# Kernel tuning notes

Hardware: AMD Instinct MI355X
Metric: run time of the kernel (lower is better)

## Reference

```python
import jax, jax.numpy as jnp
import numpy as np

B, L1, L2, D = 16, 512, 512, 512
H, INNER = 8, 1024
HD = INNER // H  # 128

def _glorot(key, shape):
    fan_in, fan_out = shape[-2], shape[-1]
    lim = jnp.sqrt(6.0 / (fan_in + fan_out))
    return jax.random.uniform(key, shape, jnp.float32, -lim, lim)

def setup_inputs() -> dict:
    key = jax.random.key(0)
    ks = jax.random.split(key, 8)
    return {
        "primary": jax.random.normal(ks[0], (B, L1, D), jnp.float32),
        "secondary": jax.random.normal(ks[1], (B, L2, D), jnp.float32),
        "primary_mask": jnp.ones((B, L1), jnp.float32),
        "secondary_mask": jnp.ones((B, L2), jnp.float32),
        "W_aff": _glorot(ks[2], (H, D, D)),          # per-head bilinear affinity weights
        "W_p": _glorot(ks[3], (D, INNER)),            # linear_primary (no bias)
        "W_s": _glorot(ks[4], (D, INNER)),            # linear_secondary (no bias)
        "W_fp": _glorot(ks[5], (D + HD, D)),          # ffn_primary
        "b_fp": jnp.zeros((D,), jnp.float32),
        "W_fs": _glorot(ks[6], (D + HD, D)),          # ffn_secondary
        "b_fs": jnp.zeros((D,), jnp.float32),
    }

def reference(primary, secondary, primary_mask, secondary_mask,
              W_aff, W_p, W_s, W_fp, b_fp, W_fs, b_fs):
    b, l1, d = primary.shape
    l2 = secondary.shape[1]
    h = W_aff.shape[0]
    hd = W_p.shape[1] // h
    # affinity mask: (B, 1, L1, L2)
    mask = (primary_mask[:, :, None] * secondary_mask[:, None, :])[:, None, :, :]
    # multi-head bilinear affinity: tanh(P Wk S^T) -> (B, H, L1, L2)
    aff = jnp.tanh(jnp.einsum('bie,hef,bjf->bhij', primary, W_aff, secondary)) * mask
    # project + split heads -> (B, H, L, hd)
    pp = (primary @ W_p).reshape(b, l1, h, hd).transpose(0, 2, 1, 3)
    ps = (secondary @ W_s).reshape(b, l2, h, hd).transpose(0, 2, 1, 3)
    # weighted sums (ReLU activation)
    wp = jax.nn.relu(jnp.einsum('bhij,bhid->bhjd', aff, pp))  # (B, H, L2, hd)
    ws = jax.nn.relu(jnp.einsum('bhij,bhjd->bhid', aff, ps))  # (B, H, L1, hd)
    # GlobalMaxPool1D applied to (L, H, hd) per sample => max over heads
    pool_p = wp.max(axis=1)  # (B, L2, hd)
    pool_s = ws.max(axis=1)  # (B, L1, hd)
    out_p = jax.nn.relu(jnp.concatenate([primary, pool_s], -1) @ W_fp + b_fp)
    out_s = jax.nn.relu(jnp.concatenate([secondary, pool_p], -1) @ W_fs + b_fs)
    return out_p, out_s
```

## Files before the change

kernel.cpp:

```cpp
#include <hip/hip_runtime.h>
#include <hip/hip_bf16.h>

typedef short short8 __attribute__((ext_vector_type(8)));
typedef float f32x16 __attribute__((ext_vector_type(16)));
typedef float f32x4 __attribute__((ext_vector_type(4)));

#define BM 128
#define BN 128

typedef const __attribute__((address_space(1))) void gas_t;
typedef __attribute__((address_space(3))) void las_t;

__device__ __forceinline__ unsigned short f2bf(float f) {
  unsigned int u = __float_as_uint(f);
  u += 0x7FFFu + ((u >> 16) & 1u);
  return (unsigned short)(u >> 16);
}

__device__ __forceinline__ float fast_tanh(float x) {
  x = fminf(fmaxf(x, -10.f), 10.f);
  float t = __builtin_amdgcn_exp2f(x * 2.8853900817779268f);
  return 1.f - 2.f * __builtin_amdgcn_rcpf(t + 1.f);
}

struct GemmP {
  const unsigned short* A;
  const unsigned short* Bm;
  void* C;
  const float* A2f;
  const unsigned short* A_b;
  const unsigned short* Bm_b;
  void* C_b;
  const float* A2f_b;
  const float* mask_p;
  const float* mask_s;
  const float* bias;
  const float* bias_b;
  long long sAb, sAh, sBb, sBh, sCb, sCh;
  int lda, lda2, ldb, ldc, M, N, K, Hh, kSplit, zSplit, nbx, nby;
};

template <int TA, int EPI>
__device__ __forceinline__ void gemm_body(const GemmP& p, int bx, int by, int bz, char* smem_) {
  constexpr int PA = (TA == 0) ? 32 : 40;
  constexpr int HSA = (TA == 0) ? 4096 : 5120;
  unsigned short* As = (unsigned short*)smem_;
  unsigned short* Bs = (unsigned short*)(smem_ + 2 * HSA * 2);

  int z = bz;
  const unsigned short* Abase = p.A;
  const unsigned short* Bbase = p.Bm;
  void* Cvp = p.C;
  const float* A2f = p.A2f;
  const float* bias = p.bias;
  if (p.zSplit && z >= p.zSplit) {
    z -= p.zSplit;
    Abase = p.A_b; Bbase = p.Bm_b; Cvp = p.C_b; A2f = p.A2f_b; bias = p.bias_b;
  }
  const int zb = z / p.Hh, zh = z % p.Hh;
  const unsigned short* A = Abase + (size_t)zb * p.sAb + (size_t)zh * p.sAh;
  const unsigned short* B = Bbase + (size_t)zb * p.sBb + (size_t)zh * p.sBh;
  const int m0 = bx * BM, n0 = by * BN;
  const int tid = threadIdx.x;
  const int wid = tid >> 6, lane = tid & 63;
  const int wm = (wid >> 1) * 64, wn = (wid & 1) * 64;
  const int lrow = lane & 31;
  const int lk8 = (lane >> 5) * 8;

  f32x16 acc[2][2] = {};

  const int dm = tid >> 2, dkg = tid & 3;

  auto mfma_block = [&]() {
#pragma unroll
    for (int h = 0; h < 2; ++h)
#pragma unroll
      for (int kc = 0; kc < 2; ++kc) {
        short8 af[2], bfv[2];
#pragma unroll
        for (int mt = 0; mt < 2; ++mt)
          af[mt] = *(const short8*)&As[h * HSA + (wm + mt * 32 + lrow) * PA + kc * 16 + lk8];
#pragma unroll
        for (int nt = 0; nt < 2; ++nt)
          bfv[nt] = *(const short8*)&Bs[h * 4096 + (wn + nt * 32 + lrow) * 32 + kc * 16 + lk8];
#pragma unroll
        for (int mt = 0; mt < 2; ++mt)
#pragma unroll
          for (int nt = 0; nt < 2; ++nt)
            acc[mt][nt] = __builtin_amdgcn_mfma_f32_32x32x16_bf16(af[mt], bfv[nt], acc[mt][nt], 0, 0, 0);
      }
  };
  auto stage_b = [&](int k0) {
#pragma unroll
    for (int h = 0; h < 2; ++h)
#pragma unroll
      for (int q = 0; q < 2; ++q) {
        const unsigned short* src = B + (size_t)(n0 + q * 64 + dm) * p.ldb + (k0 + h * 32 + dkg * 8);
        __builtin_amdgcn_global_load_lds((gas_t*)src,
                                         (las_t*)&Bs[h * 4096 + q * 2048 + wid * 512],
                                         16, 0, 0);
      }
  };

  const int nIter = p.K >> 6;
  const int nIter1 = p.kSplit ? (p.kSplit >> 6) : nIter;

  for (int it = 0; it < nIter1; ++it) {
    const int k0 = it << 6;
    if (TA == 0) {
#pragma unroll
      for (int h = 0; h < 2; ++h)
#pragma unroll
        for (int q = 0; q < 2; ++q) {
          const unsigned short* src = A + (size_t)(m0 + q * 64 + dm) * p.lda + (k0 + h * 32 + dkg * 8);
          __builtin_amdgcn_global_load_lds((gas_t*)src,
                                           (las_t*)&As[h * HSA + q * 2048 + wid * 512],
                                           16, 0, 0);
        }
    } else {
      const int kk = tid & 31, mg = (tid >> 5) << 4;
#pragma unroll
      for (int h = 0; h < 2; ++h) {
        const unsigned short* src = A + (size_t)(k0 + h * 32 + kk) * p.lda + (m0 + mg);
        uint4 v0 = *(const uint4*)src;
        uint4 v1 = *(const uint4*)(src + 8);
        unsigned short tmp[16];
        *(uint4*)&tmp[0] = v0;
        *(uint4*)&tmp[8] = v1;
#pragma unroll
        for (int j = 0; j < 16; ++j) As[h * HSA + (mg + j) * PA + kk] = tmp[j];
      }
    }
    stage_b(k0);
    __syncthreads();
    mfma_block();
    __syncthreads();
  }

  if (TA == 0 && p.kSplit) {
    for (int it = nIter1; it < nIter; ++it) {
      const int k0 = it << 6;
#pragma unroll
      for (int h = 0; h < 2; ++h) {
        const int ko = k0 + h * 32 - p.kSplit;
#pragma unroll
        for (int q = 0; q < 2; ++q) {
          const float* src = A2f + (size_t)(m0 + q * 64 + dm) * p.lda2 + (ko + dkg * 8);
          float4 v0 = *(const float4*)src;
          float4 v1 = *(const float4*)(src + 4);
          __attribute__((aligned(16))) unsigned short t[8];
          t[0] = f2bf(v0.x); t[1] = f2bf(v0.y); t[2] = f2bf(v0.z); t[3] = f2bf(v0.w);
          t[4] = f2bf(v1.x); t[5] = f2bf(v1.y); t[6] = f2bf(v1.z); t[7] = f2bf(v1.w);
          *(uint4*)&As[h * HSA + (q * 64 + dm) * 32 + dkg * 8] = *(const uint4*)t;
        }
      }
      stage_b(k0);
      __syncthreads();
      mfma_block();
      __syncthreads();
    }
  }

  unsigned short* Cu = (unsigned short*)Cvp + (size_t)zb * p.sCb + (size_t)zh * p.sCh;
  float* Cf = (float*)Cvp + (size_t)zb * p.sCb + (size_t)zh * p.sCh;

  const int rbase = 4 * (lane >> 5);

  float mp[2][16], ms[2];
  if constexpr (EPI == 1) {
#pragma unroll
    for (int mt = 0; mt < 2; ++mt)
#pragma unroll
      for (int reg = 0; reg < 16; ++reg) {
        const int rl = (reg & 3) + 8 * (reg >> 2) + rbase;
        mp[mt][reg] = p.mask_p[(size_t)zb * p.M + (m0 + wm + mt * 32 + rl)];
      }
#pragma unroll
    for (int nt = 0; nt < 2; ++nt)
      ms[nt] = p.mask_s[(size_t)zb * p.N + (n0 + wn + nt * 32 + lrow)];
  }
  if constexpr (EPI == 3) {
#pragma unroll
    for (int nt = 0; nt < 2; ++nt)
      ms[nt] = bias[n0 + wn + nt * 32 + lrow];
  }

#pragma unroll
  for (int mt = 0; mt < 2; ++mt) {
#pragma unroll
    for (int nt = 0; nt < 2; ++nt) {
      f32x16 a = acc[mt][nt];
#pragma unroll
      for (int reg = 0; reg < 16; ++reg) {
        const int rl = (reg & 3) + 8 * (reg >> 2) + rbase;
        const int grow = m0 + wm + mt * 32 + rl;
        const int gcol = n0 + wn + nt * 32 + lrow;
        const size_t idx = (size_t)grow * p.ldc + gcol;
        const float v = a[reg];
        if constexpr (EPI == 0) {
          Cu[idx] = f2bf(v);
        } else if constexpr (EPI == 1) {
          Cu[idx] = f2bf(fast_tanh(v) * (mp[mt][reg] * ms[nt]));
        } else if constexpr (EPI == 2) {
          atomicMax((int*)Cf + idx, __float_as_int(fmaxf(v, 0.f)));
        } else {
          Cf[idx] = fmaxf(v + ms[nt], 0.f);
        }
      }
    }
  }
}

template <int TA, int EPI>
__global__ __launch_bounds__(256) void gemm_k(GemmP p) {
  extern __shared__ char smem[];
  gemm_body<TA, EPI>(p, blockIdx.x, blockIdx.y, blockIdx.z, smem);
}

template <int TA1, int EPI1, int TA2, int EPI2>
__global__ __launch_bounds__(256) void gemm_pair_k(GemmP a, GemmP b, int nA) {
  extern __shared__ char smem[];
  int bid = blockIdx.x;
  if (bid < nA) {
    const int per = a.nbx * a.nby;
    const int z = bid / per, r = bid % per;
    gemm_body<TA1, EPI1>(a, r % a.nbx, r / a.nbx, z, smem);
  } else {
    bid -= nA;
    const int per = b.nbx * b.nby;
    const int z = bid / per, r = bid % per;
    gemm_body<TA2, EPI2>(b, r % b.nbx, r / b.nbx, z, smem);
  }
}

#define VMCNT6() asm volatile("s_waitcnt vmcnt(6)" ::: "memory")
#define VMCNT0() asm volatile("s_waitcnt vmcnt(0)" ::: "memory")

template <int EPI>
__device__ __forceinline__ void gemm8_body(const GemmP& p, int bx, int by, int bz, char* smem_) {
  int z = bz;
  const unsigned short* Abase = p.A;
  const unsigned short* Bbase = p.Bm;
  void* Cvp = p.C;
  if (p.zSplit && z >= p.zSplit) {
    z -= p.zSplit;
    Abase = p.A_b; Bbase = p.Bm_b; Cvp = p.C_b;
  }
  const int zb = z / p.Hh, zh = z % p.Hh;
  const unsigned short* A = Abase + (size_t)zb * p.sAb + (size_t)zh * p.sAh;
  const unsigned short* B = Bbase + (size_t)zb * p.sBb + (size_t)zh * p.sBh;
  const int m0 = bx * 256, n0 = by * 128;
  const int tid = threadIdx.x;
  const int wid = tid >> 6, lane = tid & 63;
  const int wm = wid >> 1, wn = wid & 1;
  const int lrow = lane & 15, lhi = lane >> 4;

  unsigned short* lds_u = (unsigned short*)smem_;

  const int rr = tid >> 3;
  const int cc = ((tid & 7) * 8) ^ ((rr & 7) << 3);

  const int laneA0 = (wm * 64 + lrow) * 128 + ((lhi * 16) ^ ((lrow & 7) << 4));
  const int laneB0 = (wn * 64 + lrow) * 128 + ((lhi * 16) ^ ((lrow & 7) << 4));

  f32x4 acc[4][4] = {};

  auto stageA = [&](int t, int slot) {
    const int k0 = t << 6;
    const unsigned short* s0 = A + (size_t)(m0 + rr) * p.lda + k0 + cc;
#pragma unroll
    for (int s = 0; s < 4; ++s)
      __builtin_amdgcn_global_load_lds((gas_t*)(s0 + (size_t)s * 64 * p.lda),
                                       (las_t*)(lds_u + slot * 24576 + s * 4096 + wid * 512),
                                       16, 0, 0);
  };
  auto stageB = [&](int t, int slot) {
    const int k0 = t << 6;
    const unsigned short* s0 = B + (size_t)(n0 + rr) * p.ldb + k0 + cc;
#pragma unroll
    for (int s = 0; s < 2; ++s)
      __builtin_amdgcn_global_load_lds((gas_t*)(s0 + (size_t)s * 64 * p.ldb),
                                       (las_t*)(lds_u + slot * 24576 + 16384 + s * 4096 + wid * 512),
                                       16, 0, 0);
  };

  const int nt = p.K >> 6;

  stageA(0, 0); stageB(0, 0);
  stageA(1, 1); stageB(1, 1);
  VMCNT6();
  __builtin_amdgcn_s_barrier();
  __builtin_amdgcn_sched_barrier(0);

  int slot = 0;
  for (int t = 0; t < nt; ++t) {
    const int s1 = (slot == 2) ? 0 : slot + 1;
    const int s2 = (s1 == 2) ? 0 : s1 + 1;
    const char* baseA0 = smem_ + slot * 49152 + laneA0;
    const char* baseA1 = smem_ + slot * 49152 + (laneA0 ^ 64);
    const char* baseB0 = smem_ + slot * 49152 + 32768 + laneB0;
    const char* baseB1 = smem_ + slot * 49152 + 32768 + (laneB0 ^ 64);
    short8 af[4], bv[4];

#pragma unroll
    for (int fm = 0; fm < 4; ++fm) af[fm] = *(const short8*)(baseA0 + fm * 2048);
#pragma unroll
    for (int fn = 0; fn < 4; ++fn) bv[fn] = *(const short8*)(baseB0 + fn * 2048);
    if (t + 2 < nt) stageA(t + 2, s2);
    __builtin_amdgcn_s_barrier();
    __builtin_amdgcn_sched_barrier(0);
    __builtin_amdgcn_s_setprio(1);
#pragma unroll
    for (int fm = 0; fm < 4; ++fm)
#pragma unroll
      for (int fn = 0; fn < 4; ++fn)
        acc[fm][fn] = __builtin_amdgcn_mfma_f32_16x16x32_bf16(af[fm], bv[fn], acc[fm][fn], 0, 0, 0);
    __builtin_amdgcn_s_setprio(0);
    __builtin_amdgcn_s_barrier();
    __builtin_amdgcn_sched_barrier(0);

#pragma unroll
    for (int fm = 0; fm < 4; ++fm) af[fm] = *(const short8*)(baseA1 + fm * 2048);
#pragma unroll
    for (int fn = 0; fn < 4; ++fn) bv[fn] = *(const short8*)(baseB1 + fn * 2048);
    if (t + 2 < nt) stageB(t + 2, s2);
    __builtin_amdgcn_s_barrier();
    __builtin_amdgcn_sched_barrier(0);
    __builtin_amdgcn_s_setprio(1);
#pragma unroll
    for (int fm = 0; fm < 4; ++fm)
#pragma unroll
      for (int fn = 0; fn < 4; ++fn)
        acc[fm][fn] = __builtin_amdgcn_mfma_f32_16x16x32_bf16(af[fm], bv[fn], acc[fm][fn], 0, 0, 0);
    __builtin_amdgcn_s_setprio(0);
    __builtin_amdgcn_sched_barrier(0);

    if (t + 1 < nt) {
      if (t + 2 < nt) VMCNT6(); else VMCNT0();
      __builtin_amdgcn_s_barrier();
      __builtin_amdgcn_sched_barrier(0);
    }
    slot = s1;
  }

  unsigned short* Cu = (unsigned short*)Cvp + (size_t)zb * p.sCb + (size_t)zh * p.sCh;

  float mp[4][4], ms[4];
  if constexpr (EPI == 1) {
#pragma unroll
    for (int fm = 0; fm < 4; ++fm)
#pragma unroll
      for (int reg = 0; reg < 4; ++reg)
        mp[fm][reg] = p.mask_p[(size_t)zb * p.M + (m0 + wm * 64 + fm * 16 + lhi * 4 + reg)];
#pragma unroll
    for (int fn = 0; fn < 4; ++fn)
      ms[fn] = p.mask_s[(size_t)zb * p.N + (n0 + wn * 64 + fn * 16 + lrow)];
  }

#pragma unroll
  for (int fm = 0; fm < 4; ++fm)
#pragma unroll
    for (int fn = 0; fn < 4; ++fn) {
      f32x4 a = acc[fm][fn];
      const int gcol = n0 + wn * 64 + fn * 16 + lrow;
#pragma unroll
      for (int reg = 0; reg < 4; ++reg) {
        const int grow = m0 + wm * 64 + fm * 16 + lhi * 4 + reg;
        const size_t idx = (size_t)grow * p.ldc + gcol;
        if constexpr (EPI == 0) Cu[idx] = f2bf(a[reg]);
        else                    Cu[idx] = f2bf(fast_tanh(a[reg]) * (mp[fm][reg] * ms[fn]));
      }
    }
}

template <int EPI>
__global__ __launch_bounds__(512, 2) void gemm8_k(GemmP p) {
  extern __shared__ char smem[];
  gemm8_body<EPI>(p, blockIdx.x, blockIdx.y, blockIdx.z, smem);
}

template <int E1, int E2>
__global__ __launch_bounds__(512, 2) void gemm8_pair_k(GemmP a, GemmP b, int nA) {
  extern __shared__ char smem[];
  int bid = blockIdx.x;
  if (bid < nA) {
    const int per = a.nbx * a.nby;
    const int z = bid / per, r = bid % per;
    gemm8_body<E1>(a, r % a.nbx, r / a.nbx, z, smem);
  } else {
    bid -= nA;
    const int per = b.nbx * b.nby;
    const int z = bid / per, r = bid % per;
    gemm8_body<E2>(b, r % b.nbx, r / b.nbx, z, smem);
  }
}

__device__ __forceinline__ void trans_body(const float* src, unsigned short* dst,
                                           int R, int C, int bx, int by, float (*tile)[33]) {
  const int r0 = by * 32, c0 = bx * 32;
  const int tx = threadIdx.x & 31, ty = threadIdx.x >> 5;
#pragma unroll
  for (int j = 0; j < 4; ++j)
    tile[ty + j * 8][tx] = src[(size_t)(r0 + ty + j * 8) * C + (c0 + tx)];
  __syncthreads();
#pragma unroll
  for (int j = 0; j < 4; ++j)
    dst[(size_t)(c0 + ty + j * 8) * R + (r0 + tx)] = f2bf(tile[tx][ty + j * 8]);
}

__global__ __launch_bounds__(256) void prep_k(const float* P, const float* S,
                                              unsigned short* Pbf, unsigned short* Sbf,
                                              const float* W_aff, unsigned short* WaT,
                                              const float* W_p, unsigned short* WpT,
                                              const float* W_s, unsigned short* WsT,
                                              const float* W_fp, unsigned short* WfpT,
                                              const float* W_fs, unsigned short* WfsT,
                                              float* poolz) {
  __shared__ float tile[32][33];
  const int bid = blockIdx.x;
  if (bid < 8192) {
    const int n4 = 1048576;
    int i = bid * 256 + threadIdx.x;
    const float4* s = (const float4*)P;
    ushort4* d = (ushort4*)Pbf;
    if (i >= n4) { i -= n4; s = (const float4*)S; d = (ushort4*)Sbf; }
    float4 v = s[i];
    ushort4 o;
    o.x = f2bf(v.x); o.y = f2bf(v.y); o.z = f2bf(v.z); o.w = f2bf(v.w);
    d[i] = o;
  } else if (bid < 10240) {
    const int l = bid - 8192;
    const int z = l >> 8, r = l & 255;
    trans_body(W_aff + (size_t)z * 262144, WaT + (size_t)z * 262144, 512, 512,
               r & 15, r >> 4, tile);
  } else if (bid < 11264) {
    const int l = bid - 10240;
    const int z = l >> 9, r = l & 511;
    trans_body(z ? W_s : W_p, z ? WsT : WpT, 512, 1024, r & 31, r >> 5, tile);
  } else if (bid < 11904) {
    const int l = bid - 11264;
    const int z = l / 320, r = l % 320;
    trans_body(z ? W_fs : W_fp, z ? WfsT : WfpT, 640, 512, r & 15, r >> 4, tile);
  } else {
    const int i = (bid - 11904) * 256 + threadIdx.x;
    ((float4*)poolz)[i] = float4{0.f, 0.f, 0.f, 0.f};
  }
}

extern "C" void kernel_launch(void* const* d_in, const int* in_sizes, int n_in,
                              void* d_out, int out_size, void* d_ws, size_t ws_size,
                              hipStream_t stream) {
  (void)in_sizes; (void)n_in; (void)out_size; (void)ws_size;
  const float* primary   = (const float*)d_in[0];
  const float* secondary = (const float*)d_in[1];
  const float* pmask     = (const float*)d_in[2];
  const float* smask     = (const float*)d_in[3];
  const float* W_aff     = (const float*)d_in[4];
  const float* W_p       = (const float*)d_in[5];
  const float* W_s       = (const float*)d_in[6];
  const float* W_fp      = (const float*)d_in[7];
  const float* b_fp      = (const float*)d_in[8];
  const float* W_fs      = (const float*)d_in[9];
  const float* b_fs      = (const float*)d_in[10];

  constexpr int Bb = 16, L = 512, Dd = 512, Hh = 8, HDd = 128, INNER = 1024, CAT = 640;
  constexpr int NT = Hh * Dd;
  constexpr long long LD = (long long)L * Dd;
  constexpr long long LL = (long long)L * L;

  static bool s_attr = [] {
    hipFuncSetAttribute(reinterpret_cast<const void*>(&gemm8_pair_k<0, 0>),
                        hipFuncAttributeMaxDynamicSharedMemorySize, 147456);
    hipFuncSetAttribute(reinterpret_cast<const void*>(&gemm8_k<1>),
                        hipFuncAttributeMaxDynamicSharedMemorySize, 147456);
    return true;
  }();
  (void)s_attr;

  char* base = (char*)d_ws;
  size_t off = 0;
  auto alloc = [&](size_t bytes) -> void* {
    void* r = base + off;
    off += (bytes + 255) & ~(size_t)255;
    return r;
  };

  unsigned short* Pbf   = (unsigned short*)alloc((size_t)Bb * L * Dd * 2);
  unsigned short* Sbf   = (unsigned short*)alloc((size_t)Bb * L * Dd * 2);
  unsigned short* WaT   = (unsigned short*)alloc((size_t)NT * Dd * 2);
  unsigned short* WpT   = (unsigned short*)alloc((size_t)INNER * Dd * 2);
  unsigned short* WsT   = (unsigned short*)alloc((size_t)INNER * Dd * 2);
  unsigned short* WfpT  = (unsigned short*)alloc((size_t)Dd * CAT * 2);
  unsigned short* WfsT  = (unsigned short*)alloc((size_t)Dd * CAT * 2);
  unsigned short* psT   = (unsigned short*)alloc((size_t)Bb * INNER * L * 2);
  unsigned short* ppT   = (unsigned short*)alloc((size_t)Bb * INNER * L * 2);
  unsigned short* Tbuf  = (unsigned short*)alloc((size_t)Bb * L * NT * 2);
  unsigned short* affb  = (unsigned short*)alloc((size_t)Bb * Hh * L * L * 2);
  float* pool_p = (float*)alloc((size_t)Bb * L * HDd * 4);
  float* pool_s = (float*)alloc((size_t)Bb * L * HDd * 4);

  prep_k<<<dim3(13952), dim3(256), 0, stream>>>(primary, secondary, Pbf, Sbf,
                                                W_aff, WaT, W_p, WpT, W_s, WsT,
                                                W_fp, WfpT, W_fs, WfsT, pool_p);

  {
    GemmP a{};
    a.A = Pbf; a.lda = Dd;
    a.Bm = WaT; a.ldb = Dd;
    a.C = Tbuf; a.ldc = NT;
    a.M = Bb * L; a.N = NT; a.K = Dd; a.Hh = 1; a.nbx = 32; a.nby = 32;

    GemmP b{};
    b.A = WsT; b.lda = Dd; b.sAb = 0;
    b.Bm = Sbf; b.ldb = Dd; b.sBb = LD;
    b.C = psT; b.ldc = L; b.sCb = (long long)INNER * L;
    b.A_b = WpT; b.Bm_b = Pbf; b.C_b = ppT;
    b.M = INNER; b.N = L; b.K = Dd; b.Hh = 1; b.zSplit = Bb; b.nbx = 4; b.nby = 4;

    gemm8_pair_k<0, 0><<<dim3(1024 + 512), dim3(512), 147456, stream>>>(a, b, 1024);
  }

  {
    GemmP g{};
    g.A = Tbuf; g.lda = NT; g.sAb = (long long)L * NT; g.sAh = Dd;
    g.Bm = Sbf; g.ldb = Dd; g.sBb = LD; g.sBh = 0;
    g.C = affb; g.ldc = L; g.sCb = (long long)Hh * LL; g.sCh = LL;
    g.mask_p = pmask; g.mask_s = smask;
    g.M = L; g.N = L; g.K = Dd; g.Hh = Hh;
    gemm8_k<1><<<dim3(2, 4, Bb * Hh), dim3(512), 147456, stream>>>(g);
  }

  {
    GemmP g4{};
    g4.A = affb; g4.lda = L; g4.sAb = (long long)Hh * LL; g4.sAh = LL;
    g4.Bm = psT; g4.ldb = L; g4.sBb = (long long)INNER * L; g4.sBh = (long long)HDd * L;
    g4.C = pool_s; g4.ldc = HDd; g4.sCb = (long long)L * HDd; g4.sCh = 0;
    g4.M = L; g4.N = HDd; g4.K = L; g4.Hh = Hh; g4.nbx = 4; g4.nby = 1;

    GemmP g5 = g4;
    g5.Bm = ppT;
    g5.C = pool_p;

    gemm_pair_k<0, 2, 1, 2><<<dim3(512 + 512), dim3(256), 36864, stream>>>(g4, g5, 512);
  }

  {
    GemmP g{};
    g.A = Pbf; g.lda = Dd;
    g.A2f = pool_s; g.lda2 = HDd; g.kSplit = Dd;
    g.Bm = WfpT; g.ldb = CAT;
    g.C = d_out; g.ldc = Dd;
    g.bias = b_fp;
    g.A_b = Sbf; g.A2f_b = pool_p; g.Bm_b = WfsT;
    g.C_b = (float*)d_out + (size_t)Bb * L * Dd;
    g.bias_b = b_fs;
    g.M = Bb * L; g.N = Dd; g.K = CAT; g.Hh = 1; g.zSplit = 1;
    gemm_k<0, 3><<<dim3(64, 4, 2), dim3(256), 32768, stream>>>(g);
  }
}
```

Before: 339.6 us.

## Enlarge bf16 GEMM tile to 256x256 with register-staged double-buffered LDS loads

The big bf16 GEMMs move from a 256x128 tile with triple-buffered direct global-to-LDS loads to a 256x256 tile with 8 warps in a 2x4 layout, each warp owning 128x64 of output. Global data is now loaded into registers, then written to a swizzled double-buffered LDS, so the next K-step's loads overlap the MFMAs with one block barrier per K-step. This aims to raise arithmetic intensity and cut barrier and global traffic per FLOP. In exchange it roughly doubles accumulator registers per thread, risking spills or lower occupancy, and halves the number of blocks in the grid.

```diff
diff --git a/kernel.cpp b/kernel.cpp
--- a/kernel.cpp
+++ b/kernel.cpp
@@ -233,11 +233,12 @@
   }
 }
 
-#define VMCNT6() asm volatile("s_waitcnt vmcnt(6)" ::: "memory")
-#define VMCNT0() asm volatile("s_waitcnt vmcnt(0)" ::: "memory")
+#define VMW4() asm volatile("s_waitcnt vmcnt(4)" ::: "memory")
+#define VMW0() asm volatile("s_waitcnt vmcnt(0)" ::: "memory")
+#define CBAR() asm volatile("" ::: "memory")
 
 template <int EPI>
-__device__ __forceinline__ void gemm8_body(const GemmP& p, int bx, int by, int bz, char* smem_) {
+__device__ __forceinline__ void gemm9_body(const GemmP& p, int bx, int by, int bz, char* smem_) {
   int z = bz;
   const unsigned short* Abase = p.A;
   const unsigned short* Bbase = p.Bm;
@@ -249,66 +250,67 @@
   const int zb = z / p.Hh, zh = z % p.Hh;
   const unsigned short* A = Abase + (size_t)zb * p.sAb + (size_t)zh * p.sAh;
   const unsigned short* B = Bbase + (size_t)zb * p.sBb + (size_t)zh * p.sBh;
-  const int m0 = bx * 256, n0 = by * 128;
+  const int m0 = bx * 256, n0 = by * 256;
   const int tid = threadIdx.x;
   const int wid = tid >> 6, lane = tid & 63;
-  const int wm = wid >> 1, wn = wid & 1;
+  const int wm = wid >> 2, wn = wid & 3;
   const int lrow = lane & 15, lhi = lane >> 4;
 
-  unsigned short* lds_u = (unsigned short*)smem_;
-
-  const int rr = tid >> 3;
-  const int cc = ((tid & 7) * 8) ^ ((rr & 7) << 3);
-
-  const int laneA0 = (wm * 64 + lrow) * 128 + ((lhi * 16) ^ ((lrow & 7) << 4));
-  const int laneB0 = (wn * 64 + lrow) * 128 + ((lhi * 16) ^ ((lrow & 7) << 4));
-
-  f32x4 acc[4][4] = {};
-
-  auto stageA = [&](int t, int slot) {
-    const int k0 = t << 6;
-    const unsigned short* s0 = A + (size_t)(m0 + rr) * p.lda + k0 + cc;
-#pragma unroll
-    for (int s = 0; s < 4; ++s)
-      __builtin_amdgcn_global_load_lds((gas_t*)(s0 + (size_t)s * 64 * p.lda),
-                                       (las_t*)(lds_u + slot * 24576 + s * 4096 + wid * 512),
-                                       16, 0, 0);
-  };
-  auto stageB = [&](int t, int slot) {
-    const int k0 = t << 6;
-    const unsigned short* s0 = B + (size_t)(n0 + rr) * p.ldb + k0 + cc;
-#pragma unroll
-    for (int s = 0; s < 2; ++s)
-      __builtin_amdgcn_global_load_lds((gas_t*)(s0 + (size_t)s * 64 * p.ldb),
-                                       (las_t*)(lds_u + slot * 24576 + 16384 + s * 4096 + wid * 512),
-                                       16, 0, 0);
+  unsigned short* lds = (unsigned short*)smem_;
+
+  const int srow = tid >> 1;
+  const int scS = (tid & 1) * 32;
+  const int swW = (srow & 7) << 3;
+
+  const int swr = (lrow & 7) << 4;
+  const int colA = (lhi * 16) ^ swr;
+  const int rowA0 = (wm * 128 + lrow) * 128 + colA;
+  const int rowB0 = 32768 + (wn * 64 + lrow) * 128 + colA;
+
+  f32x4 acc[8][4] = {};
+  uint4 stA[4], stB[4];
+
+  auto loadA = [&](int k0) {
+    const unsigned short* s = A + (size_t)(m0 + srow) * p.lda + k0 + scS;
+#pragma unroll
+    for (int j = 0; j < 4; ++j) stA[j] = *(const uint4*)(s + j * 8);
+    CBAR();
+  };
+  auto loadB = [&](int k0) {
+    const unsigned short* s = B + (size_t)(n0 + srow) * p.ldb + k0 + scS;
+#pragma unroll
+    for (int j = 0; j < 4; ++j) stB[j] = *(const uint4*)(s + j * 8);
+    CBAR();
+  };
+  auto writeA = [&](int other) {
+#pragma unroll
+    for (int j = 0; j < 4; ++j)
+      *(uint4*)&lds[other * 32768 + srow * 64 + ((scS + j * 8) ^ swW)] = stA[j];
+  };
+  auto writeB = [&](int other) {
+#pragma unroll
+    for (int j = 0; j < 4; ++j)
+      *(uint4*)&lds[other * 32768 + 16384 + srow * 64 + ((scS + j * 8) ^ swW)] = stB[j];
   };
 
   const int nt = p.K >> 6;
 
-  stageA(0, 0); stageB(0, 0);
-  stageA(1, 1); stageB(1, 1);
-  VMCNT6();
-  __builtin_amdgcn_s_barrier();
-  __builtin_amdgcn_sched_barrier(0);
-
-  int slot = 0;
+  loadA(0); loadB(0);
+  VMW4(); writeA(0);
+  VMW0(); writeB(0);
+  __syncthreads();
+
   for (int t = 0; t < nt; ++t) {
-    const int s1 = (slot == 2) ? 0 : slot + 1;
-    const int s2 = (s1 == 2) ? 0 : s1 + 1;
-    const char* baseA0 = smem_ + slot * 49152 + laneA0;
-    const char* baseA1 = smem_ + slot * 49152 + (laneA0 ^ 64);
-    const char* baseB0 = smem_ + slot * 49152 + 32768 + laneB0;
-    const char* baseB1 = smem_ + slot * 49152 + 32768 + (laneB0 ^ 64);
+    const int slot = t & 1, other = slot ^ 1;
+    const char* sb = smem_ + slot * 65536;
+    const int kn = (t + 1) << 6;
     short8 af[4], bv[4];
 
-#pragma unroll
-    for (int fm = 0; fm < 4; ++fm) af[fm] = *(const short8*)(baseA0 + fm * 2048);
-#pragma unroll
-    for (int fn = 0; fn < 4; ++fn) bv[fn] = *(const short8*)(baseB0 + fn * 2048);
-    if (t + 2 < nt) stageA(t + 2, s2);
-    __builtin_amdgcn_s_barrier();
-    __builtin_amdgcn_sched_barrier(0);
+    if (t + 1 < nt) loadA(kn);
+#pragma unroll
+    for (int fn = 0; fn < 4; ++fn) bv[fn] = *(const short8*)(sb + rowB0 + fn * 2048);
+#pragma unroll
+    for (int fm = 0; fm < 4; ++fm) af[fm] = *(const short8*)(sb + rowA0 + fm * 2048);
     __builtin_amdgcn_s_setprio(1);
 #pragma unroll
     for (int fm = 0; fm < 4; ++fm)
@@ -316,16 +318,23 @@
       for (int fn = 0; fn < 4; ++fn)
         acc[fm][fn] = __builtin_amdgcn_mfma_f32_16x16x32_bf16(af[fm], bv[fn], acc[fm][fn], 0, 0, 0);
     __builtin_amdgcn_s_setprio(0);
-    __builtin_amdgcn_s_barrier();
-    __builtin_amdgcn_sched_barrier(0);
-
-#pragma unroll
-    for (int fm = 0; fm < 4; ++fm) af[fm] = *(const short8*)(baseA1 + fm * 2048);
-#pragma unroll
-    for (int fn = 0; fn < 4; ++fn) bv[fn] = *(const short8*)(baseB1 + fn * 2048);
-    if (t + 2 < nt) stageB(t + 2, s2);
-    __builtin_amdgcn_s_barrier();
-    __builtin_amdgcn_sched_barrier(0);
+
+    if (t + 1 < nt) loadB(kn);
+#pragma unroll
+    for (int fm = 0; fm < 4; ++fm) af[fm] = *(const short8*)(sb + rowA0 + (4 + fm) * 2048);
+    __builtin_amdgcn_s_setprio(1);
+#pragma unroll
+    for (int fm = 0; fm < 4; ++fm)
+#pragma unroll
+      for (int fn = 0; fn < 4; ++fn)
+        acc[4 + fm][fn] = __builtin_amdgcn_mfma_f32_16x16x32_bf16(af[fm], bv[fn], acc[4 + fm][fn], 0, 0, 0);
+    __builtin_amdgcn_s_setprio(0);
+
+    if (t + 1 < nt) { VMW4(); writeA(other); }
+#pragma unroll
+    for (int fn = 0; fn < 4; ++fn) bv[fn] = *(const short8*)(sb + (rowB0 ^ 64) + fn * 2048);
+#pragma unroll
+    for (int fm = 0; fm < 4; ++fm) af[fm] = *(const short8*)(sb + (rowA0 ^ 64) + fm * 2048);
     __builtin_amdgcn_s_setprio(1);
 #pragma unroll
     for (int fm = 0; fm < 4; ++fm)
@@ -333,65 +342,69 @@
       for (int fn = 0; fn < 4; ++fn)
         acc[fm][fn] = __builtin_amdgcn_mfma_f32_16x16x32_bf16(af[fm], bv[fn], acc[fm][fn], 0, 0, 0);
     __builtin_amdgcn_s_setprio(0);
-    __builtin_amdgcn_sched_barrier(0);
-
-    if (t + 1 < nt) {
-      if (t + 2 < nt) VMCNT6(); else VMCNT0();
-      __builtin_amdgcn_s_barrier();
-      __builtin_amdgcn_sched_barrier(0);
-    }
-    slot = s1;
+
+    if (t + 1 < nt) { VMW0(); writeB(other); }
+#pragma unroll
+    for (int fm = 0; fm < 4; ++fm) af[fm] = *(const short8*)(sb + (rowA0 ^ 64) + (4 + fm) * 2048);
+    __builtin_amdgcn_s_setprio(1);
+#pragma unroll
+    for (int fm = 0; fm < 4; ++fm)
+#pragma unroll
+      for (int fn = 0; fn < 4; ++fn)
+        acc[4 + fm][fn] = __builtin_amdgcn_mfma_f32_16x16x32_bf16(af[fm], bv[fn], acc[4 + fm][fn], 0, 0, 0);
+    __builtin_amdgcn_s_setprio(0);
+
+    if (t + 1 < nt) __syncthreads();
   }
 
   unsigned short* Cu = (unsigned short*)Cvp + (size_t)zb * p.sCb + (size_t)zh * p.sCh;
 
-  float mp[4][4], ms[4];
+  float ms[4];
   if constexpr (EPI == 1) {
-#pragma unroll
-    for (int fm = 0; fm < 4; ++fm)
-#pragma unroll
-      for (int reg = 0; reg < 4; ++reg)
-        mp[fm][reg] = p.mask_p[(size_t)zb * p.M + (m0 + wm * 64 + fm * 16 + lhi * 4 + reg)];
 #pragma unroll
     for (int fn = 0; fn < 4; ++fn)
       ms[fn] = p.mask_s[(size_t)zb * p.N + (n0 + wn * 64 + fn * 16 + lrow)];
   }
 
 #pragma unroll
-  for (int fm = 0; fm < 4; ++fm)
+  for (int fm = 0; fm < 8; ++fm)
 #pragma unroll
     for (int fn = 0; fn < 4; ++fn) {
       f32x4 a = acc[fm][fn];
       const int gcol = n0 + wn * 64 + fn * 16 + lrow;
 #pragma unroll
       for (int reg = 0; reg < 4; ++reg) {
-        const int grow = m0 + wm * 64 + fm * 16 + lhi * 4 + reg;
+        const int grow = m0 + wm * 128 + fm * 16 + lhi * 4 + reg;
         const size_t idx = (size_t)grow * p.ldc + gcol;
-        if constexpr (EPI == 0) Cu[idx] = f2bf(a[reg]);
-        else                    Cu[idx] = f2bf(fast_tanh(a[reg]) * (mp[fm][reg] * ms[fn]));
+        if constexpr (EPI == 0) {
+          Cu[idx] = f2bf(a[reg]);
+        } else {
+          const float mp = p.mask_p[(size_t)zb * p.M + grow];
+          Cu[idx] = f2bf(fast_tanh(a[reg]) * (mp * ms[fn]));
+        }
       }
     }
 }
 
 template <int EPI>
-__global__ __launch_bounds__(512, 2) void gemm8_k(GemmP p) {
+__global__ __launch_bounds__(512, 2) void gemm9_k(GemmP p) {
   extern __shared__ char smem[];
-  gemm8_body<EPI>(p, blockIdx.x, blockIdx.y, blockIdx.z, smem);
+  gemm9_body<EPI>(p, blockIdx.x, blockIdx.y, blockIdx.z, smem);
 }
 
 template <int E1, int E2>
-__global__ __launch_bounds__(512, 2) void gemm8_pair_k(GemmP a, GemmP b, int nA) {
+__global__ __launch_bounds__(512, 2) void gemm9_pair_k(GemmP a, GemmP b, int nA) {
   extern __shared__ char smem[];
   int bid = blockIdx.x;
   if (bid < nA) {
     const int per = a.nbx * a.nby;
     const int z = bid / per, r = bid % per;
-    gemm8_body<E1>(a, r % a.nbx, r / a.nbx, z, smem);
+    gemm9_body<E1>(a, r % a.nbx, r / a.nbx, z, smem);
   } else {
     bid -= nA;
     const int per = b.nbx * b.nby;
     const int z = bid / per, r = bid % per;
-    gemm8_body<E2>(b, r % b.nbx, r / b.nbx, z, smem);
+    gemm9_body<E2>(b, r % b.nbx, r / b.nbx, z, smem);
   }
 }
 
@@ -469,10 +482,10 @@
   constexpr long long LL = (long long)L * L;
 
   static bool s_attr = [] {
-    hipFuncSetAttribute(reinterpret_cast<const void*>(&gemm8_pair_k<0, 0>),
-                        hipFuncAttributeMaxDynamicSharedMemorySize, 147456);
-    hipFuncSetAttribute(reinterpret_cast<const void*>(&gemm8_k<1>),
-                        hipFuncAttributeMaxDynamicSharedMemorySize, 147456);
+    hipFuncSetAttribute(reinterpret_cast<const void*>(&gemm9_pair_k<0, 0>),
+                        hipFuncAttributeMaxDynamicSharedMemorySize, 131072);
+    hipFuncSetAttribute(reinterpret_cast<const void*>(&gemm9_k<1>),
+                        hipFuncAttributeMaxDynamicSharedMemorySize, 131072);
     return true;
   }();
   (void)s_attr;
@@ -508,16 +521,16 @@
     a.A = Pbf; a.lda = Dd;
     a.Bm = WaT; a.ldb = Dd;
     a.C = Tbuf; a.ldc = NT;
-    a.M = Bb * L; a.N = NT; a.K = Dd; a.Hh = 1; a.nbx = 32; a.nby = 32;
+    a.M = Bb * L; a.N = NT; a.K = Dd; a.Hh = 1; a.nbx = 32; a.nby = 16;
 
     GemmP b{};
     b.A = WsT; b.lda = Dd; b.sAb = 0;
     b.Bm = Sbf; b.ldb = Dd; b.sBb = LD;
     b.C = psT; b.ldc = L; b.sCb = (long long)INNER * L;
     b.A_b = WpT; b.Bm_b = Pbf; b.C_b = ppT;
-    b.M = INNER; b.N = L; b.K = Dd; b.Hh = 1; b.zSplit = Bb; b.nbx = 4; b.nby = 4;
-
-    gemm8_pair_k<0, 0><<<dim3(1024 + 512), dim3(512), 147456, stream>>>(a, b, 1024);
+    b.M = INNER; b.N = L; b.K = Dd; b.Hh = 1; b.zSplit = Bb; b.nbx = 4; b.nby = 2;
+
+    gemm9_pair_k<0, 0><<<dim3(512 + 256), dim3(512), 131072, stream>>>(a, b, 512);
   }
 
   {
@@ -527,7 +540,7 @@
     g.C = affb; g.ldc = L; g.sCb = (long long)Hh * LL; g.sCh = LL;
     g.mask_p = pmask; g.mask_s = smask;
     g.M = L; g.N = L; g.K = Dd; g.Hh = Hh;
-    gemm8_k<1><<<dim3(2, 4, Bb * Hh), dim3(512), 147456, stream>>>(g);
+    gemm9_k<1><<<dim3(2, 2, Bb * Hh), dim3(512), 131072, stream>>>(g);
   }
 
   {
```

New measurement: 453.4 us. 33.5% more time.
